# Optimization experiments

Measured on AMD Instinct MI355X. Metric: run time of the kernel, lower is better.

Reference implementation:

```python
import math
import jax, jax.numpy as jnp
import numpy as np


def _procrustes_R(H):
    # H: [B, 3, 3]. Rotation R = V @ U^T with reflection fix (det(R) >= 0),
    # matching torch.svd convention (v = V, not V^T).
    u, s, vh = jnp.linalg.svd(H)
    v = jnp.swapaxes(vh, -1, -2)                       # [B,3,3]
    r = jnp.einsum('bij,bkj->bik', v, u)               # V @ U^T
    det = jnp.linalg.det(r)                            # [B]
    sign = jnp.where(det < 0, -1.0, 1.0)               # flip last column of V (reflect = diag(1,1,-1))
    flip = jnp.stack([jnp.ones_like(sign), jnp.ones_like(sign), sign], axis=-1)[:, None, :]
    v = v * flip
    return jnp.einsum('bij,bkj->bik', v, u)


def setup_inputs() -> dict:
    key = jax.random.key(0)
    k1, k2, k3, k4 = jax.random.split(key, 4)
    B, D, N, M = 8, 512, 2048, 2048
    return {
        'src_embedding': jax.random.normal(k1, (B, D, N), dtype=jnp.float32),
        'tgt_embedding': jax.random.normal(k2, (B, D, M), dtype=jnp.float32),
        'src': jax.random.normal(k3, (B, 3, N), dtype=jnp.float32),
        'tgt': jax.random.normal(k4, (B, 3, M), dtype=jnp.float32),
    }


def reference(src_embedding, tgt_embedding, src, tgt):
    d_k = src_embedding.shape[1]
    # attention correspondence: scores[b,n,m]
    scores = jnp.einsum('bdn,bdm->bnm', src_embedding, tgt_embedding) / math.sqrt(d_k)
    scores = jax.nn.softmax(scores, axis=2)
    # soft correspondence of src points in tgt: [B,3,N]
    src_corr = jnp.einsum('bdm,bnm->bdn', tgt, scores)
    src_mean = src.mean(axis=2, keepdims=True)          # [B,3,1]
    src_centered = src - src_mean
    src_corr_centered = src_corr - src_corr.mean(axis=2, keepdims=True)
    H = jnp.einsum('bin,bjn->bij', src_centered, src_corr_centered)  # [B,3,3]
    R = _procrustes_R(H)
    t = jnp.einsum('bij,bjk->bik', -R, src_mean) + tgt.mean(axis=2, keepdims=True)
    return R, t.reshape(src.shape[0], 3)
```

## Files before the change

### kernel.cpp

```cpp
#include <hip/hip_runtime.h>
#include <hip/hip_bf16.h>

#define BQ 8
#define DIM 512
#define NN 2048
#define MM 2048

typedef __attribute__((ext_vector_type(8))) short short8;
typedef __attribute__((ext_vector_type(8))) unsigned short ushort8;
typedef __attribute__((ext_vector_type(4))) float floatx4;

#define GLOAD_LDS(gp, lp) \
    __builtin_amdgcn_global_load_lds( \
        (const __attribute__((address_space(1))) void*)(gp), \
        (__attribute__((address_space(3))) void*)(lp), 16, 0, 0)


static __device__ __forceinline__ unsigned short f2bf(float x) {
    __hip_bfloat16 h = __float2bfloat16(x);
    return *(unsigned short*)&h;
}

__global__ __launch_bounds__(256, 2) void transpose_cast_kernel(
    const float* __restrict__ src_emb,
    const float* __restrict__ tgt_emb,
    __hip_bfloat16* __restrict__ Abf,
    __hip_bfloat16* __restrict__ Bbf)
{
    const int n0 = blockIdx.x * 256;
    const int d0 = blockIdx.y * 128;
    const int b  = blockIdx.z & 7;
    const int which = blockIdx.z >> 3;

    const float* in = (which == 0 ? src_emb : tgt_emb) + (size_t)b * DIM * NN;
    __hip_bfloat16* out = (which == 0 ? Abf : Bbf) + (size_t)b * NN * DIM;

    __shared__ unsigned short tl[128 * 256];

    const int t = threadIdx.x;
    const int w = t >> 6;
    const int lane = t & 63;

    #pragma unroll 8
    for (int it = 0; it < 32; it++) {
        const int dl = it * 4 + w;
        float4 v = *(const float4*)&in[(size_t)(d0 + dl) * NN + n0 + lane * 4];
        unsigned int p0 = ((unsigned)f2bf(v.y) << 16) | (unsigned)f2bf(v.x);
        unsigned int p1 = ((unsigned)f2bf(v.w) << 16) | (unsigned)f2bf(v.z);
        const int f = ((dl & 7) << 3) ^ (dl >> 3);
        *(uint2*)&tl[dl * 256 + ((lane ^ f) << 2)] = make_uint2(p0, p1);
    }
    __syncthreads();

    const int u = t & 15;
    #pragma unroll 4
    for (int pass = 0; pass < 16; pass++) {
        const int rn = (t >> 4) + pass * 16;
        ushort8 o;
        #pragma unroll
        for (int j = 0; j < 8; j++) {
            const int d = u * 8 + j;
            const int f = ((d & 7) << 3) ^ (d >> 3);
            o[j] = tl[d * 256 + (((rn >> 2) ^ f) << 2) + (rn & 3)];
        }
        *(ushort8*)&out[(size_t)(n0 + rn) * DIM + d0 + u * 8] = o;
    }
}

__global__ __launch_bounds__(256, 2) void attn_mfma_kernel(
    const __hip_bfloat16* __restrict__ Abf,
    const __hip_bfloat16* __restrict__ Bbf,
    const float* __restrict__ tgt,
    float* __restrict__ part)
{
    const int nt = blockIdx.x;
    const int qt = blockIdx.y;
    const int b  = blockIdx.z;
    const int t  = threadIdx.x;
    const int wave = t >> 6;
    const int lane = t & 63;
    const int lm   = lane & 15;
    const int quad = lane >> 4;
    const int wn   = wave * 64;

    __shared__ short As[256 * 64];
    __shared__ short Bs[128 * 64];

    const __hip_bfloat16* Abase = Abf + ((size_t)(b * NN + nt * 256)) * DIM;
    const int m0 = qt * 128;
    const __hip_bfloat16* Bbase = Bbf + ((size_t)(b * MM + m0)) * DIM;
    const float* Tb = tgt + (size_t)b * 3 * MM;

    const float SCALE = 0.044194173824159216f * 1.4426950408889634f;

    const int r8 = lane >> 3;
    const int c8 = lane & 7;
    const int cc = c8 ^ r8;
    const __hip_bfloat16* gA = Abase + (size_t)(wave * 64 + r8) * DIM + cc * 8;
    const __hip_bfloat16* gB = Bbase + (size_t)(wave * 32 + r8) * DIM + cc * 8;
    short* lA = &As[wave * 64 * 64];
    short* lB = &Bs[wave * 32 * 64];

    floatx4 acc[4][8];
    #pragma unroll
    for (int i = 0; i < 4; i++)
        #pragma unroll
        for (int j = 0; j < 8; j++)
            acc[i][j] = (floatx4){0.f, 0.f, 0.f, 0.f};

    #pragma unroll
    for (int kt = 0; kt < 8; kt++) {
        #pragma unroll
        for (int i = 0; i < 8; i++)
            GLOAD_LDS(gA + kt * 64 + (size_t)i * 8 * DIM, lA + i * 512);
        #pragma unroll
        for (int i = 0; i < 4; i++)
            GLOAD_LDS(gB + kt * 64 + (size_t)i * 8 * DIM, lB + i * 512);
        __syncthreads();

        #pragma unroll
        for (int ks = 0; ks < 2; ks++) {
            const int pc = (((ks * 4 + quad) ^ (lane & 7)) * 8);
            short8 af[4];
            #pragma unroll
            for (int i = 0; i < 4; i++)
                af[i] = *(const short8*)&As[(wn + i * 16 + lm) * 64 + pc];
            #pragma unroll
            for (int j = 0; j < 8; j++) {
                short8 bf = *(const short8*)&Bs[(j * 16 + lm) * 64 + pc];
                #pragma unroll
                for (int i = 0; i < 4; i++)
                    acc[i][j] = __builtin_amdgcn_mfma_f32_16x16x32_bf16(af[i], bf, acc[i][j], 0, 0, 0);
            }
        }
        __syncthreads();
    }

    float v0[8], v1[8], v2[8];
    #pragma unroll
    for (int j = 0; j < 8; j++) {
        int vc = m0 + j * 16 + lm;
        v0[j] = Tb[vc];
        v1[j] = Tb[MM + vc];
        v2[j] = Tb[2 * MM + vc];
    }

    const size_t slot = (size_t)(b * 16 + qt) * NN;
    #pragma unroll
    for (int i = 0; i < 4; i++) {
        float l4[4] = {0,0,0,0};
        float o0[4] = {0,0,0,0};
        float o1[4] = {0,0,0,0};
        float o2[4] = {0,0,0,0};
        #pragma unroll
        for (int j = 0; j < 8; j++) {
            #pragma unroll
            for (int r = 0; r < 4; r++) {
                float e = __builtin_amdgcn_exp2f(acc[i][j][r] * SCALE);
                l4[r] += e;
                o0[r] += e * v0[j];
                o1[r] += e * v1[j];
                o2[r] += e * v2[j];
            }
        }
        #pragma unroll
        for (int m = 1; m <= 8; m <<= 1) {
            #pragma unroll
            for (int r = 0; r < 4; r++) {
                l4[r] += __shfl_xor(l4[r], m);
                o0[r] += __shfl_xor(o0[r], m);
                o1[r] += __shfl_xor(o1[r], m);
                o2[r] += __shfl_xor(o2[r], m);
            }
        }
        if (lm == 0) {
            #pragma unroll
            for (int r = 0; r < 4; r++) {
                int n = nt * 256 + wn + i * 16 + quad * 4 + r;
                ((float4*)part)[slot + n] = make_float4(l4[r], o0[r], o1[r], o2[r]);
            }
        }
    }
}

__global__ __launch_bounds__(128) void reduce1_kernel(
    const float* __restrict__ part,
    const float* __restrict__ src,
    const float* __restrict__ tgt,
    float* __restrict__ red)
{
    const int chunk = blockIdx.x;
    const int b     = blockIdx.y;
    const int t     = threadIdx.x;
    const int n     = chunk * 128 + t;

    const float4* w4 = (const float4*)part;
    const float* S = src + (size_t)b * 3 * NN;
    const float* T = tgt + (size_t)b * 3 * MM;

    float l = 0.f, y0 = 0.f, y1 = 0.f, y2 = 0.f;
    #pragma unroll
    for (int q = 0; q < 16; q++) {
        float4 p = w4[(size_t)(b * 16 + q) * NN + n];
        l += p.x; y0 += p.y; y1 += p.z; y2 += p.w;
    }
    float inv = 1.0f / l;
    float c0 = y0 * inv, c1 = y1 * inv, c2 = y2 * inv;
    float s0 = S[n], s1 = S[NN + n], s2 = S[2 * NN + n];

    float vals[18];
    vals[0] = s0;  vals[1] = s1;  vals[2] = s2;
    vals[3] = c0;  vals[4] = c1;  vals[5] = c2;
    vals[6] = T[n]; vals[7] = T[MM + n]; vals[8] = T[2 * MM + n];
    vals[9]  = s0 * c0; vals[10] = s0 * c1; vals[11] = s0 * c2;
    vals[12] = s1 * c0; vals[13] = s1 * c1; vals[14] = s1 * c2;
    vals[15] = s2 * c0; vals[16] = s2 * c1; vals[17] = s2 * c2;

    #pragma unroll
    for (int m = 1; m <= 32; m <<= 1)
        #pragma unroll
        for (int c = 0; c < 18; c++)
            vals[c] += __shfl_xor(vals[c], m);

    __shared__ float w0[18];
    if (t == 64)
        #pragma unroll
        for (int c = 0; c < 18; c++) w0[c] = vals[c];
    __syncthreads();
    if (t == 0)
        #pragma unroll
        for (int c = 0; c < 18; c++)
            red[(size_t)(b * 16 + chunk) * 18 + c] = vals[c] + w0[c];
}

__global__ __launch_bounds__(64) void procrustes_kernel(
    const float* __restrict__ red,
    float* __restrict__ out)
{
    const int b = blockIdx.x;
    const int t = threadIdx.x;

    __shared__ float res[18];
    if (t < 18) {
        float a = 0.f;
        #pragma unroll
        for (int q = 0; q < 16; q++)
            a += red[(size_t)(b * 16 + q) * 18 + t];
        res[t] = a;
    }
    __syncthreads();

    if (t == 0) {
        const float invN = 1.0f / (float)NN;
        float mus[3], muc[3], mut[3], H[3][3];
        for (int i = 0; i < 3; i++) {
            mus[i] = res[i] * invN;
            muc[i] = res[3 + i] * invN;
            mut[i] = res[6 + i] * invN;
        }
        for (int i = 0; i < 3; i++)
            for (int j = 0; j < 3; j++)
                H[i][j] = res[9 + i * 3 + j] - (float)NN * mus[i] * muc[j];

        float A[3][3];
        for (int i = 0; i < 3; i++)
            for (int j = 0; j < 3; j++)
                A[i][j] = H[0][i] * H[0][j] + H[1][i] * H[1][j] + H[2][i] * H[2][j];

        float V[3][3] = {{1,0,0},{0,1,0},{0,0,1}};
        for (int sweep = 0; sweep < 6; sweep++) {
            for (int pi = 0; pi < 3; pi++) {
                int p = (pi < 2) ? 0 : 1;
                int q = (pi == 0) ? 1 : 2;
                float apq = A[p][q];
                if (fabsf(apq) < 1e-30f) continue;
                float tau = (A[q][q] - A[p][p]) / (2.0f * apq);
                float tt = (tau >= 0.0f) ? 1.0f / (tau + sqrtf(1.0f + tau * tau))
                                         : -1.0f / (-tau + sqrtf(1.0f + tau * tau));
                float c = 1.0f / sqrtf(1.0f + tt * tt);
                float s = tt * c;
                for (int k = 0; k < 3; k++) {
                    float akp = A[k][p], akq = A[k][q];
                    A[k][p] = c * akp - s * akq;
                    A[k][q] = s * akp + c * akq;
                }
                for (int k = 0; k < 3; k++) {
                    float apk = A[p][k], aqk = A[q][k];
                    A[p][k] = c * apk - s * aqk;
                    A[q][k] = s * apk + c * aqk;
                }
                for (int k = 0; k < 3; k++) {
                    float vkp = V[k][p], vkq = V[k][q];
                    V[k][p] = c * vkp - s * vkq;
                    V[k][q] = s * vkp + c * vkq;
                }
            }
        }

        float lam[3] = {A[0][0], A[1][1], A[2][2]};
        int idx[3] = {0, 1, 2};
        for (int a = 0; a < 2; a++)
            for (int bb = 0; bb < 2 - a; bb++)
                if (lam[idx[bb]] < lam[idx[bb + 1]]) { int tmp = idx[bb]; idx[bb] = idx[bb + 1]; idx[bb + 1] = tmp; }

        float Vc[3][3], U[3][3];
        for (int c = 0; c < 3; c++) {
            float sv = sqrtf(fmaxf(lam[idx[c]], 0.0f));
            float isv = 1.0f / fmaxf(sv, 1e-20f);
            for (int r = 0; r < 3; r++) {
                Vc[r][c] = V[r][idx[c]];
                U[r][c] = (H[r][0] * V[0][idx[c]] + H[r][1] * V[1][idx[c]] + H[r][2] * V[2][idx[c]]) * isv;
            }
        }

        {
            float nrm = rsqrtf(U[0][0]*U[0][0] + U[1][0]*U[1][0] + U[2][0]*U[2][0]);
            for (int r = 0; r < 3; r++) U[r][0] *= nrm;
            float d01 = U[0][0]*U[0][1] + U[1][0]*U[1][1] + U[2][0]*U[2][1];
            for (int r = 0; r < 3; r++) U[r][1] -= d01 * U[r][0];
            nrm = rsqrtf(U[0][1]*U[0][1] + U[1][1]*U[1][1] + U[2][1]*U[2][1]);
            for (int r = 0; r < 3; r++) U[r][1] *= nrm;
            float d02 = U[0][0]*U[0][2] + U[1][0]*U[1][2] + U[2][0]*U[2][2];
            float d12 = U[0][1]*U[0][2] + U[1][1]*U[1][2] + U[2][1]*U[2][2];
            for (int r = 0; r < 3; r++) U[r][2] -= d02 * U[r][0] + d12 * U[r][1];
            nrm = rsqrtf(U[0][2]*U[0][2] + U[1][2]*U[1][2] + U[2][2]*U[2][2]);
            for (int r = 0; r < 3; r++) U[r][2] *= nrm;
        }

        float det = H[0][0]*(H[1][1]*H[2][2] - H[1][2]*H[2][1])
                  - H[0][1]*(H[1][0]*H[2][2] - H[1][2]*H[2][0])
                  + H[0][2]*(H[1][0]*H[2][1] - H[1][1]*H[2][0]);
        float sgn = (det < 0.0f) ? -1.0f : 1.0f;

        float R[3][3];
        for (int i = 0; i < 3; i++)
            for (int j = 0; j < 3; j++)
                R[i][j] = Vc[i][0]*U[j][0] + Vc[i][1]*U[j][1] + sgn * Vc[i][2]*U[j][2];

        for (int i = 0; i < 3; i++)
            for (int j = 0; j < 3; j++)
                out[b * 9 + i * 3 + j] = R[i][j];
        for (int i = 0; i < 3; i++)
            out[BQ * 9 + b * 3 + i] = mut[i] - (R[i][0]*mus[0] + R[i][1]*mus[1] + R[i][2]*mus[2]);
    }
}

extern "C" void kernel_launch(void* const* d_in, const int* in_sizes, int n_in,
                              void* d_out, int out_size, void* d_ws, size_t ws_size,
                              hipStream_t stream) {
    const float* src_emb = (const float*)d_in[0];
    const float* tgt_emb = (const float*)d_in[1];
    const float* src     = (const float*)d_in[2];
    const float* tgt     = (const float*)d_in[3];
    float* out = (float*)d_out;

    float* part = (float*)d_ws;
    __hip_bfloat16* Abf = (__hip_bfloat16*)((char*)d_ws + (4 << 20));
    __hip_bfloat16* Bbf = (__hip_bfloat16*)((char*)d_ws + (20 << 20));
    float* red = (float*)((char*)d_ws + (36 << 20));

    dim3 gridT(NN / 256, DIM / 128, 2 * BQ);
    transpose_cast_kernel<<<gridT, 256, 0, stream>>>(src_emb, tgt_emb, Abf, Bbf);

    dim3 gridA(NN / 256, MM / 128, BQ);
    attn_mfma_kernel<<<gridA, 256, 0, stream>>>(Abf, Bbf, tgt, part);

    dim3 gridR(16, BQ);
    reduce1_kernel<<<gridR, 128, 0, stream>>>(part, src, tgt, red);

    procrustes_kernel<<<BQ, 64, 0, stream>>>(red, out);
}
```

Before: 159.2 us.

## Fuse reduction and Procrustes solve into attention kernel via last-block ticket

Removes the separate reduce1 and procrustes kernels. Each attention block increments a per-batch atomic ticket after a threadfence, and the last of the 128 blocks for a batch performs the full reduction over N and the 3x3 SVD solve. This saves two kernel launches and the intermediate round trip through global memory. In exchange it adds a memset launch, and the final reduction now runs serially in one block per batch.

```diff
diff --git a/kernel.cpp b/kernel.cpp
--- a/kernel.cpp
+++ b/kernel.cpp
@@ -70,8 +70,11 @@
 __global__ __launch_bounds__(256, 2) void attn_mfma_kernel(
     const __hip_bfloat16* __restrict__ Abf,
     const __hip_bfloat16* __restrict__ Bbf,
+    const float* __restrict__ src,
     const float* __restrict__ tgt,
-    float* __restrict__ part)
+    float* __restrict__ part,
+    unsigned int* __restrict__ ticket,
+    float* __restrict__ out)
 {
     const int nt = blockIdx.x;
     const int qt = blockIdx.y;
@@ -181,167 +184,154 @@
             }
         }
     }
-}
-
-__global__ __launch_bounds__(128) void reduce1_kernel(
-    const float* __restrict__ part,
-    const float* __restrict__ src,
-    const float* __restrict__ tgt,
-    float* __restrict__ red)
-{
-    const int chunk = blockIdx.x;
-    const int b     = blockIdx.y;
-    const int t     = threadIdx.x;
-    const int n     = chunk * 128 + t;
-
-    const float4* w4 = (const float4*)part;
-    const float* S = src + (size_t)b * 3 * NN;
-    const float* T = tgt + (size_t)b * 3 * MM;
-
-    float l = 0.f, y0 = 0.f, y1 = 0.f, y2 = 0.f;
-    #pragma unroll
-    for (int q = 0; q < 16; q++) {
-        float4 p = w4[(size_t)(b * 16 + q) * NN + n];
-        l += p.x; y0 += p.y; y1 += p.z; y2 += p.w;
-    }
-    float inv = 1.0f / l;
-    float c0 = y0 * inv, c1 = y1 * inv, c2 = y2 * inv;
-    float s0 = S[n], s1 = S[NN + n], s2 = S[2 * NN + n];
-
-    float vals[18];
-    vals[0] = s0;  vals[1] = s1;  vals[2] = s2;
-    vals[3] = c0;  vals[4] = c1;  vals[5] = c2;
-    vals[6] = T[n]; vals[7] = T[MM + n]; vals[8] = T[2 * MM + n];
-    vals[9]  = s0 * c0; vals[10] = s0 * c1; vals[11] = s0 * c2;
-    vals[12] = s1 * c0; vals[13] = s1 * c1; vals[14] = s1 * c2;
-    vals[15] = s2 * c0; vals[16] = s2 * c1; vals[17] = s2 * c2;
-
-    #pragma unroll
-    for (int m = 1; m <= 32; m <<= 1)
-        #pragma unroll
-        for (int c = 0; c < 18; c++)
-            vals[c] += __shfl_xor(vals[c], m);
-
-    __shared__ float w0[18];
-    if (t == 64)
-        #pragma unroll
-        for (int c = 0; c < 18; c++) w0[c] = vals[c];
+
+    __threadfence();
     __syncthreads();
-    if (t == 0)
-        #pragma unroll
-        for (int c = 0; c < 18; c++)
-            red[(size_t)(b * 16 + chunk) * 18 + c] = vals[c] + w0[c];
-}
-
-__global__ __launch_bounds__(64) void procrustes_kernel(
-    const float* __restrict__ red,
-    float* __restrict__ out)
-{
-    const int b = blockIdx.x;
-    const int t = threadIdx.x;
-
-    __shared__ float res[18];
-    if (t < 18) {
-        float a = 0.f;
-        #pragma unroll
-        for (int q = 0; q < 16; q++)
-            a += red[(size_t)(b * 16 + q) * 18 + t];
-        res[t] = a;
-    }
+    __shared__ unsigned int sTicket;
+    if (t == 0) sTicket = atomicAdd(&ticket[b], 1u);
     __syncthreads();
-
-    if (t == 0) {
-        const float invN = 1.0f / (float)NN;
-        float mus[3], muc[3], mut[3], H[3][3];
-        for (int i = 0; i < 3; i++) {
-            mus[i] = res[i] * invN;
-            muc[i] = res[3 + i] * invN;
-            mut[i] = res[6 + i] * invN;
-        }
-        for (int i = 0; i < 3; i++)
-            for (int j = 0; j < 3; j++)
-                H[i][j] = res[9 + i * 3 + j] - (float)NN * mus[i] * muc[j];
-
-        float A[3][3];
-        for (int i = 0; i < 3; i++)
-            for (int j = 0; j < 3; j++)
-                A[i][j] = H[0][i] * H[0][j] + H[1][i] * H[1][j] + H[2][i] * H[2][j];
-
-        float V[3][3] = {{1,0,0},{0,1,0},{0,0,1}};
-        for (int sweep = 0; sweep < 6; sweep++) {
-            for (int pi = 0; pi < 3; pi++) {
-                int p = (pi < 2) ? 0 : 1;
-                int q = (pi == 0) ? 1 : 2;
-                float apq = A[p][q];
-                if (fabsf(apq) < 1e-30f) continue;
-                float tau = (A[q][q] - A[p][p]) / (2.0f * apq);
-                float tt = (tau >= 0.0f) ? 1.0f / (tau + sqrtf(1.0f + tau * tau))
-                                         : -1.0f / (-tau + sqrtf(1.0f + tau * tau));
-                float c = 1.0f / sqrtf(1.0f + tt * tt);
-                float s = tt * c;
-                for (int k = 0; k < 3; k++) {
-                    float akp = A[k][p], akq = A[k][q];
-                    A[k][p] = c * akp - s * akq;
-                    A[k][q] = s * akp + c * akq;
+    if (sTicket != 127u) return;
+    __threadfence();
+
+    {
+        const float4* w4 = (const float4*)part;
+        const float* S = src + (size_t)b * 3 * NN;
+        const float* T = tgt + (size_t)b * 3 * MM;
+
+        float vals[18];
+        #pragma unroll
+        for (int c = 0; c < 18; c++) vals[c] = 0.f;
+
+        for (int k = 0; k < 8; k++) {
+            const int n = t + k * 256;
+            float l = 0.f, y0 = 0.f, y1 = 0.f, y2 = 0.f;
+            #pragma unroll
+            for (int q = 0; q < 16; q++) {
+                float4 p = w4[(size_t)(b * 16 + q) * NN + n];
+                l += p.x; y0 += p.y; y1 += p.z; y2 += p.w;
+            }
+            float inv = 1.0f / l;
+            float c0 = y0 * inv, c1 = y1 * inv, c2 = y2 * inv;
+            float s0 = S[n], s1 = S[NN + n], s2 = S[2 * NN + n];
+
+            vals[0] += s0;  vals[1] += s1;  vals[2] += s2;
+            vals[3] += c0;  vals[4] += c1;  vals[5] += c2;
+            vals[6] += T[n]; vals[7] += T[MM + n]; vals[8] += T[2 * MM + n];
+            vals[9]  += s0 * c0; vals[10] += s0 * c1; vals[11] += s0 * c2;
+            vals[12] += s1 * c0; vals[13] += s1 * c1; vals[14] += s1 * c2;
+            vals[15] += s2 * c0; vals[16] += s2 * c1; vals[17] += s2 * c2;
+        }
+
+        #pragma unroll
+        for (int m = 1; m <= 32; m <<= 1)
+            #pragma unroll
+            for (int c = 0; c < 18; c++)
+                vals[c] += __shfl_xor(vals[c], m);
+
+        __shared__ float wsum[4][18];
+        if (lane == 0)
+            #pragma unroll
+            for (int c = 0; c < 18; c++) wsum[wave][c] = vals[c];
+        __syncthreads();
+
+        if (t == 0) {
+            float res[18];
+            #pragma unroll
+            for (int c = 0; c < 18; c++)
+                res[c] = wsum[0][c] + wsum[1][c] + wsum[2][c] + wsum[3][c];
+
+            const float invN = 1.0f / (float)NN;
+            float mus[3], muc[3], mut[3], H[3][3];
+            for (int i = 0; i < 3; i++) {
+                mus[i] = res[i] * invN;
+                muc[i] = res[3 + i] * invN;
+                mut[i] = res[6 + i] * invN;
+            }
+            for (int i = 0; i < 3; i++)
+                for (int j = 0; j < 3; j++)
+                    H[i][j] = res[9 + i * 3 + j] - (float)NN * mus[i] * muc[j];
+
+            float A[3][3];
+            for (int i = 0; i < 3; i++)
+                for (int j = 0; j < 3; j++)
+                    A[i][j] = H[0][i] * H[0][j] + H[1][i] * H[1][j] + H[2][i] * H[2][j];
+
+            float V[3][3] = {{1,0,0},{0,1,0},{0,0,1}};
+            for (int sweep = 0; sweep < 6; sweep++) {
+                for (int pi = 0; pi < 3; pi++) {
+                    int p = (pi < 2) ? 0 : 1;
+                    int q = (pi == 0) ? 1 : 2;
+                    float apq = A[p][q];
+                    if (fabsf(apq) < 1e-30f) continue;
+                    float tau = (A[q][q] - A[p][p]) / (2.0f * apq);
+                    float tt = (tau >= 0.0f) ? 1.0f / (tau + sqrtf(1.0f + tau * tau))
+                                             : -1.0f / (-tau + sqrtf(1.0f + tau * tau));
+                    float c = 1.0f / sqrtf(1.0f + tt * tt);
+                    float s = tt * c;
+                    for (int k = 0; k < 3; k++) {
+                        float akp = A[k][p], akq = A[k][q];
+                        A[k][p] = c * akp - s * akq;
+                        A[k][q] = s * akp + c * akq;
+                    }
+                    for (int k = 0; k < 3; k++) {
+                        float apk = A[p][k], aqk = A[q][k];
+                        A[p][k] = c * apk - s * aqk;
+                        A[q][k] = s * apk + c * aqk;
+                    }
+                    for (int k = 0; k < 3; k++) {
+                        float vkp = V[k][p], vkq = V[k][q];
+                        V[k][p] = c * vkp - s * vkq;
+                        V[k][q] = s * vkp + c * vkq;
+                    }
                 }
-                for (int k = 0; k < 3; k++) {
-                    float apk = A[p][k], aqk = A[q][k];
-                    A[p][k] = c * apk - s * aqk;
-                    A[q][k] = s * apk + c * aqk;
+            }
+
+            float lam[3] = {A[0][0], A[1][1], A[2][2]};
+            int idx[3] = {0, 1, 2};
+            for (int a = 0; a < 2; a++)
+                for (int bb = 0; bb < 2 - a; bb++)
+                    if (lam[idx[bb]] < lam[idx[bb + 1]]) { int tmp = idx[bb]; idx[bb] = idx[bb + 1]; idx[bb + 1] = tmp; }
+
+            float Vc[3][3], U[3][3];
+            for (int c = 0; c < 3; c++) {
+                float sv = sqrtf(fmaxf(lam[idx[c]], 0.0f));
+                float isv = 1.0f / fmaxf(sv, 1e-20f);
+                for (int r = 0; r < 3; r++) {
+                    Vc[r][c] = V[r][idx[c]];
+                    U[r][c] = (H[r][0] * V[0][idx[c]] + H[r][1] * V[1][idx[c]] + H[r][2] * V[2][idx[c]]) * isv;
                 }
-                for (int k = 0; k < 3; k++) {
-                    float vkp = V[k][p], vkq = V[k][q];
-                    V[k][p] = c * vkp - s * vkq;
-                    V[k][q] = s * vkp + c * vkq;
-                }
-            }
-        }
-
-        float lam[3] = {A[0][0], A[1][1], A[2][2]};
-        int idx[3] = {0, 1, 2};
-        for (int a = 0; a < 2; a++)
-            for (int bb = 0; bb < 2 - a; bb++)
-                if (lam[idx[bb]] < lam[idx[bb + 1]]) { int tmp = idx[bb]; idx[bb] = idx[bb + 1]; idx[bb + 1] = tmp; }
-
-        float Vc[3][3], U[3][3];
-        for (int c = 0; c < 3; c++) {
-            float sv = sqrtf(fmaxf(lam[idx[c]], 0.0f));
-            float isv = 1.0f / fmaxf(sv, 1e-20f);
-            for (int r = 0; r < 3; r++) {
-                Vc[r][c] = V[r][idx[c]];
-                U[r][c] = (H[r][0] * V[0][idx[c]] + H[r][1] * V[1][idx[c]] + H[r][2] * V[2][idx[c]]) * isv;
-            }
-        }
-
-        {
-            float nrm = rsqrtf(U[0][0]*U[0][0] + U[1][0]*U[1][0] + U[2][0]*U[2][0]);
-            for (int r = 0; r < 3; r++) U[r][0] *= nrm;
-            float d01 = U[0][0]*U[0][1] + U[1][0]*U[1][1] + U[2][0]*U[2][1];
-            for (int r = 0; r < 3; r++) U[r][1] -= d01 * U[r][0];
-            nrm = rsqrtf(U[0][1]*U[0][1] + U[1][1]*U[1][1] + U[2][1]*U[2][1]);
-            for (int r = 0; r < 3; r++) U[r][1] *= nrm;
-            float d02 = U[0][0]*U[0][2] + U[1][0]*U[1][2] + U[2][0]*U[2][2];
-            float d12 = U[0][1]*U[0][2] + U[1][1]*U[1][2] + U[2][1]*U[2][2];
-            for (int r = 0; r < 3; r++) U[r][2] -= d02 * U[r][0] + d12 * U[r][1];
-            nrm = rsqrtf(U[0][2]*U[0][2] + U[1][2]*U[1][2] + U[2][2]*U[2][2]);
-            for (int r = 0; r < 3; r++) U[r][2] *= nrm;
-        }
-
-        float det = H[0][0]*(H[1][1]*H[2][2] - H[1][2]*H[2][1])
-                  - H[0][1]*(H[1][0]*H[2][2] - H[1][2]*H[2][0])
-                  + H[0][2]*(H[1][0]*H[2][1] - H[1][1]*H[2][0]);
-        float sgn = (det < 0.0f) ? -1.0f : 1.0f;
-
-        float R[3][3];
-        for (int i = 0; i < 3; i++)
-            for (int j = 0; j < 3; j++)
-                R[i][j] = Vc[i][0]*U[j][0] + Vc[i][1]*U[j][1] + sgn * Vc[i][2]*U[j][2];
-
-        for (int i = 0; i < 3; i++)
-            for (int j = 0; j < 3; j++)
-                out[b * 9 + i * 3 + j] = R[i][j];
-        for (int i = 0; i < 3; i++)
-            out[BQ * 9 + b * 3 + i] = mut[i] - (R[i][0]*mus[0] + R[i][1]*mus[1] + R[i][2]*mus[2]);
+            }
+
+            {
+                float nrm = rsqrtf(U[0][0]*U[0][0] + U[1][0]*U[1][0] + U[2][0]*U[2][0]);
+                for (int r = 0; r < 3; r++) U[r][0] *= nrm;
+                float d01 = U[0][0]*U[0][1] + U[1][0]*U[1][1] + U[2][0]*U[2][1];
+                for (int r = 0; r < 3; r++) U[r][1] -= d01 * U[r][0];
+                nrm = rsqrtf(U[0][1]*U[0][1] + U[1][1]*U[1][1] + U[2][1]*U[2][1]);
+                for (int r = 0; r < 3; r++) U[r][1] *= nrm;
+                float d02 = U[0][0]*U[0][2] + U[1][0]*U[1][2] + U[2][0]*U[2][2];
+                float d12 = U[0][1]*U[0][2] + U[1][1]*U[1][2] + U[2][1]*U[2][2];
+                for (int r = 0; r < 3; r++) U[r][2] -= d02 * U[r][0] + d12 * U[r][1];
+                nrm = rsqrtf(U[0][2]*U[0][2] + U[1][2]*U[1][2] + U[2][2]*U[2][2]);
+                for (int r = 0; r < 3; r++) U[r][2] *= nrm;
+            }
+
+            float det = H[0][0]*(H[1][1]*H[2][2] - H[1][2]*H[2][1])
+                      - H[0][1]*(H[1][0]*H[2][2] - H[1][2]*H[2][0])
+                      + H[0][2]*(H[1][0]*H[2][1] - H[1][1]*H[2][0]);
+            float sgn = (det < 0.0f) ? -1.0f : 1.0f;
+
+            float R[3][3];
+            for (int i = 0; i < 3; i++)
+                for (int j = 0; j < 3; j++)
+                    R[i][j] = Vc[i][0]*U[j][0] + Vc[i][1]*U[j][1] + sgn * Vc[i][2]*U[j][2];
+
+            for (int i = 0; i < 3; i++)
+                for (int j = 0; j < 3; j++)
+                    out[b * 9 + i * 3 + j] = R[i][j];
+            for (int i = 0; i < 3; i++)
+                out[BQ * 9 + b * 3 + i] = mut[i] - (R[i][0]*mus[0] + R[i][1]*mus[1] + R[i][2]*mus[2]);
+        }
     }
 }
 
@@ -357,16 +347,13 @@
     float* part = (float*)d_ws;
     __hip_bfloat16* Abf = (__hip_bfloat16*)((char*)d_ws + (4 << 20));
     __hip_bfloat16* Bbf = (__hip_bfloat16*)((char*)d_ws + (20 << 20));
-    float* red = (float*)((char*)d_ws + (36 << 20));
+    unsigned int* ticket = (unsigned int*)((char*)d_ws + (36 << 20));
+
+    hipMemsetAsync(ticket, 0, 8 * sizeof(unsigned int), stream);
 
     dim3 gridT(NN / 256, DIM / 128, 2 * BQ);
     transpose_cast_kernel<<<gridT, 256, 0, stream>>>(src_emb, tgt_emb, Abf, Bbf);
 
     dim3 gridA(NN / 256, MM / 128, BQ);
-    attn_mfma_kernel<<<gridA, 256, 0, stream>>>(Abf, Bbf, tgt, part);
-
-    dim3 gridR(16, BQ);
-    reduce1_kernel<<<gridR, 128, 0, stream>>>(part, src, tgt, red);
-
-    procrustes_kernel<<<BQ, 64, 0, stream>>>(red, out);
+    attn_mfma_kernel<<<gridA, 256, 0, stream>>>(Abf, Bbf, src, tgt, part, ticket, out);
 }
```

Result: slower. 276.0 us (+73.3%).
